# Optimization experiments

Measured on AMD Instinct MI355X. Metric: run time of the kernel, lower is better.

The kernel has to match this reference:

```python
import jax, jax.numpy as jnp
import numpy as np
from jax import lax

# dims: T steps, B batch, V vocab, E embed, H hidden, N cache slots, DK key dim, DV value dim
T, B, V, E, H, N, DK, DV = 64, 32, 32000, 512, 512, 512, 256, 512


def setup_inputs() -> dict:
    key = jax.random.key(0)
    ks = jax.random.split(key, 12)
    rn = lambda i, shape, scale: jax.random.normal(ks[i], shape, jnp.float32) * scale
    return {
        "tokens": jax.random.randint(ks[0], (T, B), 0, V),
        "emb": rn(1, (V, E), 0.02),
        "Wq": rn(2, (E, DK), E ** -0.5),
        "Wk": rn(3, (E, DK), E ** -0.5),
        "Wv": rn(4, (H, DV), H ** -0.5),
        "Wh": rn(5, (E + DV, H), (E + DV) ** -0.5),
        "bh": jnp.zeros((H,), jnp.float32),
        "Wout": rn(6, (H, V), H ** -0.5),
        "bout": jnp.zeros((V,), jnp.float32),
        "keys0": rn(7, (N, DK), 0.02),
        "values0": rn(8, (N, DV), 0.02),
        "k": 8,
    }


def reference(tokens, emb, Wq, Wk, Wv, Wh, bh, Wout, bout, keys0, values0, k):
    scale = 1.0 / jnp.sqrt(jnp.float32(DK))

    def step(carry, tok_t):
        keys, vals, ptr = carry
        x = emb[tok_t]                                  # [B, E] embedding gather
        q = x @ Wq                                      # [B, DK]
        scores = (q @ keys.T) * scale                   # [B, N]
        top_s, top_i = lax.top_k(scores, k)             # [B, k]
        w = jax.nn.softmax(top_s, axis=-1)              # [B, k]
        v_sel = vals[top_i]                             # [B, k, DV] irregular gather
        retrieved = jnp.einsum('bk,bkd->bd', w, v_sel)  # [B, DV]
        h = jnp.tanh(jnp.concatenate([x, retrieved], axis=-1) @ Wh + bh)  # [B, H]
        # circular-pointer cache write (batch-pooled key/value)
        new_key = jnp.mean(x @ Wk, axis=0)              # [DK]
        new_val = jnp.mean(h @ Wv, axis=0)              # [DV]
        keys = lax.dynamic_update_slice(keys, new_key[None, :], (ptr, 0))
        vals = lax.dynamic_update_slice(vals, new_val[None, :], (ptr, 0))
        ptr = (ptr + 1) % N
        return (keys, vals, ptr), h

    init = (keys0, values0, jnp.int32(0))
    _, hiddens = lax.scan(step, init, tokens)           # [T, B, H]
    logits = hiddens @ Wout + bout                      # [T, B, V]
    return logits
```

## Files before the change

kernel.cpp:

```cpp
#include <hip/hip_runtime.h>

typedef _Float16 half_t;
typedef _Float16 half8 __attribute__((ext_vector_type(8)));
typedef float f32x4 __attribute__((ext_vector_type(4)));


__device__ __forceinline__ void gload_lds16(const void* g, void* l) {
  __builtin_amdgcn_global_load_lds((const __attribute__((address_space(1))) void*)g,
                                   (__attribute__((address_space(3))) void*)l, 16, 0, 0);
}

__device__ __forceinline__ void prepTile(int pid, const float* __restrict__ Wout,
                                         half_t* __restrict__ WoutT,
                                         const float* __restrict__ Wh,
                                         half_t* __restrict__ W1T,
                                         half_t* __restrict__ W2T,
                                         char* smem) {
  half_t (*tile)[68] = (half_t(*)[68])smem;
  if (pid < 4000) {
    int n0 = (pid % 500) * 64, k0 = (pid / 500) * 64;
    for (int p = 0; p < 4; p++) {
      int id = p * 256 + threadIdx.x;
      int k = id >> 4, nq = id & 15;
      float4 v = *(const float4*)&Wout[(size_t)(k0 + k) * 32000 + n0 + nq * 4];
      tile[nq * 4 + 0][k] = (half_t)v.x; tile[nq * 4 + 1][k] = (half_t)v.y;
      tile[nq * 4 + 2][k] = (half_t)v.z; tile[nq * 4 + 3][k] = (half_t)v.w;
    }
    __syncthreads();
    for (int p = 0; p < 2; p++) {
      int id = p * 256 + threadIdx.x;
      int n = id >> 3, kc = id & 7;
      half8 h = *(const half8*)&tile[n][kc * 8];
      *(half8*)&WoutT[(size_t)(n0 + n) * 512 + k0 + kc * 8] = h;
    }
  } else {
    int id2 = pid - 4000;
    int n0 = (id2 & 7) * 64, k0 = (id2 >> 3) * 64;
    for (int p = 0; p < 16; p++) {
      int id = p * 256 + threadIdx.x;
      int kk = id >> 6, nn = id & 63;
      tile[nn][kk] = (half_t)Wh[(size_t)(k0 + kk) * 512 + n0 + nn];
    }
    __syncthreads();
    half_t* out = (k0 < 512) ? W1T : W2T;
    int kb = k0 & 511;
    for (int p = 0; p < 16; p++) {
      int id = p * 256 + threadIdx.x;
      int nn = id >> 6, kk = id & 63;
      out[(size_t)(n0 + nn) * 512 + kb + kk] = tile[nn][kk];
    }
  }
}

__global__ __launch_bounds__(256) void kGE(const int* __restrict__ tok,
                                           const float* __restrict__ emb,
                                           const float* __restrict__ Wq,
                                           const float* __restrict__ Wk,
                                           double* __restrict__ Qd,
                                           float* __restrict__ Q32,
                                           half_t* __restrict__ Xh,
                                           double* __restrict__ NKd,
                                           float* __restrict__ NKf) {
  __shared__ __align__(16) char smem[8192];
  int bid = blockIdx.x, tid = threadIdx.x;
  if (bid < 512) {
    float (*xs)[512] = (float(*)[512])smem;
    int r0 = bid * 4;
    for (int rr = 0; rr < 4; rr++) {
      int row = r0 + rr;
      const float* src = emb + (size_t)tok[row] * 512;
      float v0 = src[tid], v1 = src[tid + 256];
      xs[rr][tid] = v0; xs[rr][tid + 256] = v1;
      Xh[(size_t)row * 512 + tid] = (half_t)v0;
      Xh[(size_t)row * 512 + tid + 256] = (half_t)v1;
    }
    __syncthreads();
    int d = tid;
    double a0 = 0, a1 = 0, a2 = 0, a3 = 0;
    #pragma unroll 4
    for (int i = 0; i < 512; i++) {
      double w = (double)Wq[(size_t)i * 256 + d];
      a0 += (double)xs[0][i] * w; a1 += (double)xs[1][i] * w;
      a2 += (double)xs[2][i] * w; a3 += (double)xs[3][i] * w;
    }
    Qd[(size_t)(r0 + 0) * 256 + d] = a0; Qd[(size_t)(r0 + 1) * 256 + d] = a1;
    Qd[(size_t)(r0 + 2) * 256 + d] = a2; Qd[(size_t)(r0 + 3) * 256 + d] = a3;
    Q32[(size_t)(r0 + 0) * 256 + d] = (float)a0; Q32[(size_t)(r0 + 1) * 256 + d] = (float)a1;
    Q32[(size_t)(r0 + 2) * 256 + d] = (float)a2; Q32[(size_t)(r0 + 3) * 256 + d] = (float)a3;
  } else {
    double* xm = (double*)smem;
    int bid2 = bid - 512, t = bid2 >> 3, ch = bid2 & 7;
    int c = tid;
    double s0 = 0.0, s1 = 0.0;
    for (int b = 0; b < 32; b++) {
      const float* src = emb + (size_t)tok[t * 32 + b] * 512;
      s0 += (double)src[c]; s1 += (double)src[c + 256];
    }
    xm[c] = s0 * (1.0 / 32.0);
    xm[c + 256] = s1 * (1.0 / 32.0);
    __syncthreads();
    if (tid < 32) {
      int d = ch * 32 + tid;
      double a = 0;
      #pragma unroll 4
      for (int i = 0; i < 512; i++) a += xm[i] * (double)Wk[(size_t)i * 256 + d];
      NKd[(size_t)t * 256 + d] = a;
      NKf[(size_t)t * 256 + d] = (float)a;
    }
  }
}

__global__ __launch_bounds__(256) void kSP(const float* __restrict__ Q32,
                                           const float* __restrict__ keys0,
                                           const float* __restrict__ NKf,
                                           float* __restrict__ S,
                                           const float* __restrict__ Wout,
                                           half_t* __restrict__ WoutT,
                                           const float* __restrict__ Wh,
                                           half_t* __restrict__ W1T,
                                           half_t* __restrict__ W2T,
                                           int* __restrict__ DEP,
                                           int* __restrict__ bars) {
  __shared__ __align__(16) char smem[17408];
  int b = blockIdx.x, tid = threadIdx.x;
  if (b < 288) {
    float (*As)[68] = (float(*)[68])smem;
    float (*Bs)[68] = (float(*)[68])(smem + 8704);
    int m0 = (b & 31) * 64, n0 = (b >> 5) * 64;
    int tx = tid & 15, ty = tid >> 4;
    float acc[4][4];
    #pragma unroll
    for (int i = 0; i < 4; i++)
      #pragma unroll
      for (int j = 0; j < 4; j++) acc[i][j] = 0.f;
    for (int kc = 0; kc < 256; kc += 32) {
      __syncthreads();
      #pragma unroll
      for (int p = 0; p < 8; p++) {
        int idx = p * 256 + tid;
        int k = idx & 31, m = idx >> 5;
        As[k][m] = Q32[(size_t)(m0 + m) * 256 + kc + k];
        int n = n0 + m;
        Bs[k][m] = (n < 512) ? keys0[(size_t)n * 256 + kc + k]
                             : NKf[(size_t)(n - 512) * 256 + kc + k];
      }
      __syncthreads();
      #pragma unroll
      for (int k = 0; k < 32; k++) {
        float4 a = *(const float4*)&As[k][ty * 4];
        float4 bb = *(const float4*)&Bs[k][tx * 4];
        acc[0][0] += a.x * bb.x; acc[0][1] += a.x * bb.y; acc[0][2] += a.x * bb.z; acc[0][3] += a.x * bb.w;
        acc[1][0] += a.y * bb.x; acc[1][1] += a.y * bb.y; acc[1][2] += a.y * bb.z; acc[1][3] += a.y * bb.w;
        acc[2][0] += a.z * bb.x; acc[2][1] += a.z * bb.y; acc[2][2] += a.z * bb.z; acc[2][3] += a.z * bb.w;
        acc[3][0] += a.w * bb.x; acc[3][1] += a.w * bb.y; acc[3][2] += a.w * bb.z; acc[3][3] += a.w * bb.w;
      }
    }
    #pragma unroll
    for (int i = 0; i < 4; i++) {
      float4 o = {acc[i][0], acc[i][1], acc[i][2], acc[i][3]};
      *(float4*)&S[(size_t)(m0 + ty * 4 + i) * 576 + n0 + tx * 4] = o;
    }
  } else if (b < 2288) {
    prepTile(b - 288, Wout, WoutT, Wh, W1T, W2T, smem);
  } else {
    if (tid < 64) DEP[tid] = 0;
    bars[tid] = 0;
  }
}

__global__ __launch_bounds__(256) void kTR(const float* __restrict__ S,
                                           const double* __restrict__ Qd,
                                           const double* __restrict__ NKd,
                                           const float* __restrict__ keys0,
                                           const float* __restrict__ vals0,
                                           float* __restrict__ WSo,
                                           int* __restrict__ ISo,
                                           half_t* __restrict__ R16,
                                           int* __restrict__ DEP,
                                           const float* __restrict__ Wout,
                                           half_t* __restrict__ WoutT,
                                           const float* __restrict__ Wh,
                                           half_t* __restrict__ W1T,
                                           half_t* __restrict__ W2T) {
  __shared__ __align__(16) char smem[8704];
  int bid = blockIdx.x, tid = threadIdx.x;
  if (bid >= 512) {
    prepTile(2000 + (bid - 512), Wout, WoutT, Wh, W1T, W2T, smem);
    return;
  }
  __shared__ float wls[4][8];
  __shared__ int ils[4][8];
  __shared__ int depf;
  if (tid == 0) depf = 0;
  __syncthreads();
  int r0b = bid * 4;
  int wv = tid >> 6, lane = tid & 63;
  int row = r0b + wv;
  int t = row >> 5;
  const float* Srow = S + (size_t)row * 576;
  float v[8];
  #pragma unroll
  for (int j = 0; j < 8; j++) v[j] = Srow[j * 64 + lane];
  if (lane < t) v[0] = Srow[512 + lane];
  int ci[12];
  #pragma unroll
  for (int it = 0; it < 12; it++) {
    float bv = -1e30f; int bi = 0x7fffffff;
    #pragma unroll
    for (int j = 0; j < 8; j++) {
      int ii = j * 64 + lane;
      if (v[j] > bv || (v[j] == bv && ii < bi)) { bv = v[j]; bi = ii; }
    }
    #pragma unroll
    for (int s = 32; s > 0; s >>= 1) {
      float ov = __shfl_xor(bv, s, 64);
      int oi = __shfl_xor(bi, s, 64);
      if (ov > bv || (ov == bv && oi < bi)) { bv = ov; bi = oi; }
    }
    ci[it] = bi;
    #pragma unroll
    for (int j = 0; j < 8; j++)
      if (j * 64 + lane == bi) v[j] = -1e30f;
  }
  const double* qrow = Qd + (size_t)row * 256 + lane * 4;
  double q0 = qrow[0], q1 = qrow[1], q2 = qrow[2], q3 = qrow[3];
  double dv[12];
  #pragma unroll
  for (int c = 0; c < 12; c++) {
    int idx = ci[c];
    double p;
    if (idx < t) {
      const double* kr = NKd + (size_t)idx * 256 + lane * 4;
      p = q0 * kr[0] + q1 * kr[1] + q2 * kr[2] + q3 * kr[3];
    } else {
      const float* kr = keys0 + (size_t)idx * 256 + lane * 4;
      p = q0 * (double)kr[0] + q1 * (double)kr[1] + q2 * (double)kr[2] + q3 * (double)kr[3];
    }
    #pragma unroll
    for (int s = 32; s > 0; s >>= 1) p += __shfl_xor(p, s, 64);
    dv[c] = p * 0.0625;
  }
  double tv[8]; int ti[8];
  #pragma unroll
  for (int it = 0; it < 8; it++) {
    double bv = -1e300; int bi = 0x7fffffff;
    #pragma unroll
    for (int c = 0; c < 12; c++)
      if (dv[c] > bv || (dv[c] == bv && ci[c] < bi)) { bv = dv[c]; bi = ci[c]; }
    tv[it] = bv; ti[it] = bi;
    #pragma unroll
    for (int c = 0; c < 12; c++)
      if (ci[c] == bi) dv[c] = -1e300;
  }
  if (lane == 0) {
    double m = tv[0], ev[8], Z = 0;
    #pragma unroll
    for (int i2 = 0; i2 < 8; i2++) { ev[i2] = exp(tv[i2] - m); Z += ev[i2]; }
    double inv = 1.0 / Z;
    int dep = 0;
    #pragma unroll
    for (int i2 = 0; i2 < 8; i2++) {
      float w = (float)(ev[i2] * inv);
      WSo[(size_t)row * 8 + i2] = w;
      ISo[(size_t)row * 8 + i2] = ti[i2];
      wls[wv][i2] = w; ils[wv][i2] = ti[i2];
      if (ti[i2] < t) dep = 1;
    }
    if (dep) atomicOr(&depf, 1);
  }
  __syncthreads();
  if (tid == 0 && depf) atomicOr(&DEP[t], 1);
  for (int rr = 0; rr < 4; rr++) {
    float a0 = 0.f, a1 = 0.f;
    #pragma unroll
    for (int k2 = 0; k2 < 8; k2++) {
      const float* src = vals0 + (size_t)ils[rr][k2] * 512;
      a0 += wls[rr][k2] * src[tid];
      a1 += wls[rr][k2] * src[tid + 256];
    }
    R16[(size_t)(r0b + rr) * 512 + tid] = (half_t)a0;
    R16[(size_t)(r0b + rr) * 512 + tid + 256] = (half_t)a1;
  }
}

__device__ __forceinline__ void gbar(int* bars, int id, int nwg) {
  __syncthreads();
  if (threadIdx.x == 0) {
    __hip_atomic_fetch_add(&bars[id], 1, __ATOMIC_ACQ_REL, __HIP_MEMORY_SCOPE_AGENT);
    while (__hip_atomic_load(&bars[id], __ATOMIC_ACQUIRE, __HIP_MEMORY_SCOPE_AGENT) < nwg)
      __builtin_amdgcn_s_sleep(4);
  }
  __syncthreads();
}

__global__ __launch_bounds__(256) void kH(const half_t* __restrict__ Xh,
                                          const half_t* __restrict__ R16,
                                          const half_t* __restrict__ W1T,
                                          const half_t* __restrict__ W2T,
                                          const float* __restrict__ bh,
                                          const float* __restrict__ Wv,
                                          float* __restrict__ XH,
                                          half_t* __restrict__ HH,
                                          float* __restrict__ HM,
                                          float* __restrict__ NV,
                                          int* __restrict__ bars) {
  __shared__ half_t lA[3][64 * 32];
  __shared__ half_t lB[3][64 * 32];
  __shared__ float hmld[512];
  int b = blockIdx.x;
  int m0 = (b >> 3) * 64, n0 = (b & 7) * 64;
  int tid = threadIdx.x, wid = tid >> 6, lane = tid & 63;
  int wm = wid >> 1, wn = wid & 1;
  f32x4 acc[2][2];
  #pragma unroll
  for (int i = 0; i < 2; i++)
    #pragma unroll
    for (int j = 0; j < 2; j++) acc[i][j] = (f32x4){0.f, 0.f, 0.f, 0.f};
  int rA = lane >> 2;
  int cswz = ((lane & 3) ^ ((lane >> 3) & 3)) * 8;
  int koffs = (((lane >> 4) ^ ((lane >> 1) & 3))) * 8;
  auto issue = [&](int j, int buf) {
    const half_t* Ap = (j < 16) ? Xh : R16;
    const half_t* Bp = (j < 16) ? W1T : W2T;
    int kk = j & 15;
    gload_lds16(Ap + ((size_t)(m0 + wid * 16 + rA) * 512 + kk * 32 + cswz), (void*)(&lA[buf][wid * 512]));
    gload_lds16(Bp + ((size_t)(n0 + wid * 16 + rA) * 512 + kk * 32 + cswz), (void*)(&lB[buf][wid * 512]));
  };
  issue(0, 0); issue(1, 1);
  for (int kt = 0; kt < 32; kt++) {
    if (kt < 31) asm volatile("s_waitcnt vmcnt(2)\n\ts_barrier" ::: "memory");
    else         asm volatile("s_waitcnt vmcnt(0)\n\ts_barrier" ::: "memory");
    int cur = kt % 3;
    half8 af[2], bf[2];
    #pragma unroll
    for (int mf = 0; mf < 2; mf++)
      af[mf] = *(const half8*)&lA[cur][(wm * 32 + mf * 16 + (lane & 15)) * 32 + koffs];
    #pragma unroll
    for (int nf = 0; nf < 2; nf++)
      bf[nf] = *(const half8*)&lB[cur][(wn * 32 + nf * 16 + (lane & 15)) * 32 + koffs];
    if (kt < 30) issue(kt + 2, (kt + 2) % 3);
    #pragma unroll
    for (int mf = 0; mf < 2; mf++)
      #pragma unroll
      for (int nf = 0; nf < 2; nf++)
        acc[mf][nf] = __builtin_amdgcn_mfma_f32_16x16x32_f16(af[mf], bf[nf], acc[mf][nf], 0, 0, 0);
    if (kt == 15) {
      #pragma unroll
      for (int nf = 0; nf < 2; nf++) {
        int col = n0 + wn * 32 + nf * 16 + (lane & 15);
        float bv = bh[col];
        #pragma unroll
        for (int mf = 0; mf < 2; mf++) {
          int rbase = m0 + wm * 32 + mf * 16 + (lane >> 4) * 4;
          #pragma unroll
          for (int r = 0; r < 4; r++)
            XH[(size_t)(rbase + r) * 512 + col] = acc[mf][nf][r] + bv;
        }
      }
    }
  }
  #pragma unroll
  for (int nf = 0; nf < 2; nf++) {
    int col = n0 + wn * 32 + nf * 16 + (lane & 15);
    float bv = bh[col];
    float cs = 0.f;
    #pragma unroll
    for (int mf = 0; mf < 2; mf++) {
      int rbase = m0 + wm * 32 + mf * 16 + (lane >> 4) * 4;
      #pragma unroll
      for (int r = 0; r < 4; r++) {
        float v = tanhf(acc[mf][nf][r] + bv);
        HH[(size_t)(rbase + r) * 512 + col] = (half_t)v;
        cs += v;
      }
    }
    cs += __shfl_xor(cs, 16, 64);
    cs += __shfl_xor(cs, 32, 64);
    if ((lane >> 4) == 0) {
      int t = (m0 >> 5) + wm;
      HM[(size_t)t * 512 + col] = cs * (1.f / 32.f);
    }
  }
  gbar(bars, 0, 256);
  int t2 = b >> 2, ch = b & 3;
  hmld[tid] = HM[(size_t)t2 * 512 + tid];
  hmld[tid + 256] = HM[(size_t)t2 * 512 + tid + 256];
  __syncthreads();
  if (tid < 128) {
    int col = ch * 128 + tid;
    float a = 0.f;
    #pragma unroll 4
    for (int i = 0; i < 512; i++) a += hmld[i] * Wv[(size_t)i * 512 + col];
    NV[(size_t)t2 * 512 + col] = a;
  }
}

__global__ __launch_bounds__(256) void kFixup(const int* __restrict__ DEP,
                                              int* __restrict__ bars,
                                              const float* __restrict__ XHm,
                                              const float* __restrict__ Wh,
                                              const float* __restrict__ Wv,
                                              const float* __restrict__ vals0,
                                              const float* __restrict__ WSo,
                                              const int* __restrict__ ISo,
                                              float* __restrict__ NV,
                                              float* __restrict__ RETR,
                                              float* __restrict__ HB,
                                              half_t* __restrict__ HHm) {
  __shared__ float rl[512];
  __shared__ float hm2[512];
  int w = blockIdx.x;
  int barid = 0;
  for (int t = 0; t < 64; t++) {
    if (DEP[t] == 0) continue;
    {
      int b = w >> 1, hf = w & 1;
      int c = hf * 256 + threadIdx.x;
      int row = t * 32 + b;
      float acc = 0.f;
      #pragma unroll
      for (int k2 = 0; k2 < 8; k2++) {
        int idx = ISo[(size_t)row * 8 + k2];
        float wv2 = WSo[(size_t)row * 8 + k2];
        const float* src = (idx < t) ? (NV + (size_t)idx * 512) : (vals0 + (size_t)idx * 512);
        acc += wv2 * src[c];
      }
      RETR[(size_t)b * 512 + c] = acc;
    }
    gbar(bars, barid++, 64);
    if (w < 32) {
      int b = w;
      rl[threadIdx.x] = RETR[(size_t)b * 512 + threadIdx.x];
      rl[threadIdx.x + 256] = RETR[(size_t)b * 512 + threadIdx.x + 256];
      __syncthreads();
      int row = t * 32 + b;
      for (int cc = 0; cc < 2; cc++) {
        int col = cc * 256 + threadIdx.x;
        float acc = 0.f;
        #pragma unroll 4
        for (int i = 0; i < 512; i++) acc += rl[i] * Wh[(size_t)(512 + i) * 512 + col];
        float h = tanhf(XHm[(size_t)row * 512 + col] + acc);
        HB[(size_t)b * 512 + col] = h;
        HHm[(size_t)row * 512 + col] = (half_t)h;
      }
    }
    gbar(bars, barid++, 64);
    if (w == 0) {
      for (int j = threadIdx.x; j < 512; j += 256) {
        float s = 0.f;
        for (int b = 0; b < 32; b++) s += HB[(size_t)b * 512 + j];
        hm2[j] = s * (1.f / 32.f);
      }
      __syncthreads();
      for (int v = threadIdx.x; v < 512; v += 256) {
        float a = 0.f;
        #pragma unroll 4
        for (int i = 0; i < 512; i++) a += hm2[i] * Wv[(size_t)i * 512 + v];
        NV[(size_t)t * 512 + v] = a;
      }
    }
    gbar(bars, barid++, 64);
  }
}

__global__ __launch_bounds__(256) void kLogits(const half_t* __restrict__ A,
                                               const half_t* __restrict__ Bm,
                                               const float* __restrict__ bout,
                                               float* __restrict__ C) {
  __shared__ half_t lA[3][128 * 32];
  __shared__ half_t lB[3][128 * 32];
  int lin = blockIdx.y * 250 + blockIdx.x;
  int swz = (lin & 7) * 500 + (lin >> 3);
  int m0 = (swz & 15) * 128;
  int n0 = (swz >> 4) * 128;
  int tid = threadIdx.x, wid = tid >> 6, lane = tid & 63;
  int wm = wid >> 1, wn = wid & 1;
  f32x4 acc[4][4];
  #pragma unroll
  for (int a2 = 0; a2 < 4; a2++)
    #pragma unroll
    for (int b2 = 0; b2 < 4; b2++) acc[a2][b2] = (f32x4){0.f, 0.f, 0.f, 0.f};
  int rA = lane >> 2;
  int cswz = ((lane & 3) ^ ((lane >> 3) & 3)) * 8;
  int koffs = (((lane >> 4) ^ ((lane >> 1) & 3))) * 8;
  auto issue = [&](int j, int buf) {
    #pragma unroll
    for (int i2 = 0; i2 < 2; i2++) {
      int blk = wid * 2 + i2;
      gload_lds16(A + ((size_t)(m0 + blk * 16 + rA) * 512 + j * 32 + cswz), (void*)(&lA[buf][blk * 512]));
      gload_lds16(Bm + ((size_t)(n0 + blk * 16 + rA) * 512 + j * 32 + cswz), (void*)(&lB[buf][blk * 512]));
    }
  };
  issue(0, 0); issue(1, 1);
  for (int kt = 0; kt < 16; kt++) {
    if (kt < 15) asm volatile("s_waitcnt vmcnt(4)\n\ts_barrier" ::: "memory");
    else         asm volatile("s_waitcnt vmcnt(0)\n\ts_barrier" ::: "memory");
    int cur = kt % 3;
    half8 af[4], bf[4];
    #pragma unroll
    for (int mf = 0; mf < 4; mf++)
      af[mf] = *(const half8*)&lA[cur][(wm * 64 + mf * 16 + (lane & 15)) * 32 + koffs];
    #pragma unroll
    for (int nf = 0; nf < 4; nf++)
      bf[nf] = *(const half8*)&lB[cur][(wn * 64 + nf * 16 + (lane & 15)) * 32 + koffs];
    if (kt < 14) issue(kt + 2, (kt + 2) % 3);
    #pragma unroll
    for (int mf = 0; mf < 4; mf++)
      #pragma unroll
      for (int nf = 0; nf < 4; nf++)
        acc[mf][nf] = __builtin_amdgcn_mfma_f32_16x16x32_f16(af[mf], bf[nf], acc[mf][nf], 0, 0, 0);
  }
  #pragma unroll
  for (int nf = 0; nf < 4; nf++) {
    int col = n0 + wn * 64 + nf * 16 + (lane & 15);
    float bv = bout[col];
    #pragma unroll
    for (int mf = 0; mf < 4; mf++) {
      int rbase = m0 + wm * 64 + mf * 16 + (lane >> 4) * 4;
      #pragma unroll
      for (int r = 0; r < 4; r++)
        C[(size_t)(rbase + r) * 32000 + col] = acc[mf][nf][r] + bv;
    }
  }
}

extern "C" void kernel_launch(void* const* d_in, const int* in_sizes, int n_in,
                              void* d_out, int out_size, void* d_ws, size_t ws_size,
                              hipStream_t stream) {
  (void)in_sizes; (void)n_in; (void)out_size; (void)ws_size;
  const int*   tok   = (const int*)d_in[0];
  const float* emb   = (const float*)d_in[1];
  const float* Wq    = (const float*)d_in[2];
  const float* Wk    = (const float*)d_in[3];
  const float* Wv    = (const float*)d_in[4];
  const float* Wh    = (const float*)d_in[5];
  const float* bh    = (const float*)d_in[6];
  const float* Wout  = (const float*)d_in[7];
  const float* bout  = (const float*)d_in[8];
  const float* keys0 = (const float*)d_in[9];
  const float* vals0 = (const float*)d_in[10];
  float* Cout = (float*)d_out;

  char* ws = (char*)d_ws;
  size_t off = 0;
  auto alloc = [&](size_t bytes) -> char* {
    char* p = ws + off;
    off += (bytes + 255) & ~(size_t)255;
    return p;
  };
  half_t* WoutT = (half_t*)alloc(32768000);
  half_t* W1T   = (half_t*)alloc(524288);
  half_t* W2T   = (half_t*)alloc(524288);
  half_t* Xh    = (half_t*)alloc(2097152);
  double* Qd    = (double*)alloc(4194304);
  float*  Q32   = (float*) alloc(2097152);
  double* NKd   = (double*)alloc(131072);
  float*  NKf   = (float*) alloc(65536);
  float*  Sb    = (float*) alloc(4718592);
  float*  XH    = (float*) alloc(4194304);
  float*  WSb   = (float*) alloc(65536);
  int*    ISb   = (int*)   alloc(65536);
  float*  NV    = (float*) alloc(131072);
  half_t* R16   = (half_t*)alloc(2097152);
  half_t* HH    = (half_t*)alloc(2097152);
  float*  HM    = (float*) alloc(131072);
  float*  RETR  = (float*) alloc(65536);
  float*  HB    = (float*) alloc(65536);
  int*    DEP   = (int*)   alloc(256);
  int*    bars  = (int*)   alloc(1024);

  kGE<<<1024, 256, 0, stream>>>(tok, emb, Wq, Wk, Qd, Q32, Xh, NKd, NKf);
  kSP<<<2289, 256, 0, stream>>>(Q32, keys0, NKf, Sb, Wout, WoutT, Wh, W1T, W2T, DEP, bars);
  kTR<<<2640, 256, 0, stream>>>(Sb, Qd, NKd, keys0, vals0, WSb, ISb, R16, DEP,
                                Wout, WoutT, Wh, W1T, W2T);
  kH<<<256, 256, 0, stream>>>(Xh, R16, W1T, W2T, bh, Wv, XH, HH, HM, NV, bars);
  kFixup<<<64, 256, 0, stream>>>(DEP, bars + 16, XH, Wh, Wv, vals0, WSb, ISb, NV, RETR, HB, HH);
  kLogits<<<dim3(250, 16), 256, 0, stream>>>(HH, WoutT, bout, Cout);
}
```

Before: 328.0 us.

## Move all weight prep into first kernel and stage logits epilogue through LDS

All weight transpose/convert tiles (Wout, Wh) and the DEP/bars reset now run as extra blocks of the first embedding kernel instead of being spread across the score and top-k kernels, which shrink to just their real work. The logits GEMM epilogue now writes accumulators into LDS in two halves and then emits coalesced float4 stores with a vectorised bias add, replacing scattered scalar stores. This rebalances the work across kernels and improves store coalescing on the largest output, at the cost of extra barriers and LDS traffic in the epilogue. It also puts the prep work into one large front-loaded grid.

```diff
diff --git a/kernel.cpp b/kernel.cpp
--- a/kernel.cpp
+++ b/kernel.cpp
@@ -60,9 +60,21 @@
                                            float* __restrict__ Q32,
                                            half_t* __restrict__ Xh,
                                            double* __restrict__ NKd,
-                                           float* __restrict__ NKf) {
-  __shared__ __align__(16) char smem[8192];
+                                           float* __restrict__ NKf,
+                                           const float* __restrict__ Wout,
+                                           half_t* __restrict__ WoutT,
+                                           const float* __restrict__ Wh,
+                                           half_t* __restrict__ W1T,
+                                           half_t* __restrict__ W2T,
+                                           int* __restrict__ DEP,
+                                           int* __restrict__ bars) {
+  __shared__ __align__(16) char smem[8704];
   int bid = blockIdx.x, tid = threadIdx.x;
+  if (bid >= 1024) {
+    if (bid < 5152) prepTile(bid - 1024, Wout, WoutT, Wh, W1T, W2T, smem);
+    else { if (tid < 64) DEP[tid] = 0; bars[tid] = 0; }
+    return;
+  }
   if (bid < 512) {
     float (*xs)[512] = (float(*)[512])smem;
     int r0 = bid * 4;
@@ -110,61 +122,46 @@
   }
 }
 
-__global__ __launch_bounds__(256) void kSP(const float* __restrict__ Q32,
-                                           const float* __restrict__ keys0,
-                                           const float* __restrict__ NKf,
-                                           float* __restrict__ S,
-                                           const float* __restrict__ Wout,
-                                           half_t* __restrict__ WoutT,
-                                           const float* __restrict__ Wh,
-                                           half_t* __restrict__ W1T,
-                                           half_t* __restrict__ W2T,
-                                           int* __restrict__ DEP,
-                                           int* __restrict__ bars) {
-  __shared__ __align__(16) char smem[17408];
+__global__ __launch_bounds__(256) void kS(const float* __restrict__ Q32,
+                                          const float* __restrict__ keys0,
+                                          const float* __restrict__ NKf,
+                                          float* __restrict__ S) {
+  __shared__ float As[32][68];
+  __shared__ float Bs[32][68];
   int b = blockIdx.x, tid = threadIdx.x;
-  if (b < 288) {
-    float (*As)[68] = (float(*)[68])smem;
-    float (*Bs)[68] = (float(*)[68])(smem + 8704);
-    int m0 = (b & 31) * 64, n0 = (b >> 5) * 64;
-    int tx = tid & 15, ty = tid >> 4;
-    float acc[4][4];
-    #pragma unroll
-    for (int i = 0; i < 4; i++)
-      #pragma unroll
-      for (int j = 0; j < 4; j++) acc[i][j] = 0.f;
-    for (int kc = 0; kc < 256; kc += 32) {
-      __syncthreads();
-      #pragma unroll
-      for (int p = 0; p < 8; p++) {
-        int idx = p * 256 + tid;
-        int k = idx & 31, m = idx >> 5;
-        As[k][m] = Q32[(size_t)(m0 + m) * 256 + kc + k];
-        int n = n0 + m;
-        Bs[k][m] = (n < 512) ? keys0[(size_t)n * 256 + kc + k]
-                             : NKf[(size_t)(n - 512) * 256 + kc + k];
-      }
-      __syncthreads();
-      #pragma unroll
-      for (int k = 0; k < 32; k++) {
-        float4 a = *(const float4*)&As[k][ty * 4];
-        float4 bb = *(const float4*)&Bs[k][tx * 4];
-        acc[0][0] += a.x * bb.x; acc[0][1] += a.x * bb.y; acc[0][2] += a.x * bb.z; acc[0][3] += a.x * bb.w;
-        acc[1][0] += a.y * bb.x; acc[1][1] += a.y * bb.y; acc[1][2] += a.y * bb.z; acc[1][3] += a.y * bb.w;
-        acc[2][0] += a.z * bb.x; acc[2][1] += a.z * bb.y; acc[2][2] += a.z * bb.z; acc[2][3] += a.z * bb.w;
-        acc[3][0] += a.w * bb.x; acc[3][1] += a.w * bb.y; acc[3][2] += a.w * bb.z; acc[3][3] += a.w * bb.w;
-      }
-    }
-    #pragma unroll
-    for (int i = 0; i < 4; i++) {
-      float4 o = {acc[i][0], acc[i][1], acc[i][2], acc[i][3]};
-      *(float4*)&S[(size_t)(m0 + ty * 4 + i) * 576 + n0 + tx * 4] = o;
-    }
-  } else if (b < 2288) {
-    prepTile(b - 288, Wout, WoutT, Wh, W1T, W2T, smem);
-  } else {
-    if (tid < 64) DEP[tid] = 0;
-    bars[tid] = 0;
+  int m0 = (b & 31) * 64, n0 = (b >> 5) * 64;
+  int tx = tid & 15, ty = tid >> 4;
+  float acc[4][4];
+  #pragma unroll
+  for (int i = 0; i < 4; i++)
+    #pragma unroll
+    for (int j = 0; j < 4; j++) acc[i][j] = 0.f;
+  for (int kc = 0; kc < 256; kc += 32) {
+    __syncthreads();
+    #pragma unroll
+    for (int p = 0; p < 8; p++) {
+      int idx = p * 256 + tid;
+      int k = idx & 31, m = idx >> 5;
+      As[k][m] = Q32[(size_t)(m0 + m) * 256 + kc + k];
+      int n = n0 + m;
+      Bs[k][m] = (n < 512) ? keys0[(size_t)n * 256 + kc + k]
+                           : NKf[(size_t)(n - 512) * 256 + kc + k];
+    }
+    __syncthreads();
+    #pragma unroll
+    for (int k = 0; k < 32; k++) {
+      float4 a = *(const float4*)&As[k][ty * 4];
+      float4 bb = *(const float4*)&Bs[k][tx * 4];
+      acc[0][0] += a.x * bb.x; acc[0][1] += a.x * bb.y; acc[0][2] += a.x * bb.z; acc[0][3] += a.x * bb.w;
+      acc[1][0] += a.y * bb.x; acc[1][1] += a.y * bb.y; acc[1][2] += a.y * bb.z; acc[1][3] += a.y * bb.w;
+      acc[2][0] += a.z * bb.x; acc[2][1] += a.z * bb.y; acc[2][2] += a.z * bb.z; acc[2][3] += a.z * bb.w;
+      acc[3][0] += a.w * bb.x; acc[3][1] += a.w * bb.y; acc[3][2] += a.w * bb.z; acc[3][3] += a.w * bb.w;
+    }
+  }
+  #pragma unroll
+  for (int i = 0; i < 4; i++) {
+    float4 o = {acc[i][0], acc[i][1], acc[i][2], acc[i][3]};
+    *(float4*)&S[(size_t)(m0 + ty * 4 + i) * 576 + n0 + tx * 4] = o;
   }
 }
 
@@ -176,21 +173,11 @@
                                            float* __restrict__ WSo,
                                            int* __restrict__ ISo,
                                            half_t* __restrict__ R16,
-                                           int* __restrict__ DEP,
-                                           const float* __restrict__ Wout,
-                                           half_t* __restrict__ WoutT,
-                                           const float* __restrict__ Wh,
-                                           half_t* __restrict__ W1T,
-                                           half_t* __restrict__ W2T) {
-  __shared__ __align__(16) char smem[8704];
-  int bid = blockIdx.x, tid = threadIdx.x;
-  if (bid >= 512) {
-    prepTile(2000 + (bid - 512), Wout, WoutT, Wh, W1T, W2T, smem);
-    return;
-  }
+                                           int* __restrict__ DEP) {
   __shared__ float wls[4][8];
   __shared__ int ils[4][8];
   __shared__ int depf;
+  int bid = blockIdx.x, tid = threadIdx.x;
   if (tid == 0) depf = 0;
   __syncthreads();
   int r0b = bid * 4;
@@ -467,8 +454,9 @@
                                                const half_t* __restrict__ Bm,
                                                const float* __restrict__ bout,
                                                float* __restrict__ C) {
-  __shared__ half_t lA[3][128 * 32];
-  __shared__ half_t lB[3][128 * 32];
+  __shared__ __align__(16) char smem[49152];
+  half_t* lAb = (half_t*)smem;
+  half_t* lBb = (half_t*)(smem + 24576);
   int lin = blockIdx.y * 250 + blockIdx.x;
   int swz = (lin & 7) * 500 + (lin >> 3);
   int m0 = (swz & 15) * 128;
@@ -487,8 +475,8 @@
     #pragma unroll
     for (int i2 = 0; i2 < 2; i2++) {
       int blk = wid * 2 + i2;
-      gload_lds16(A + ((size_t)(m0 + blk * 16 + rA) * 512 + j * 32 + cswz), (void*)(&lA[buf][blk * 512]));
-      gload_lds16(Bm + ((size_t)(n0 + blk * 16 + rA) * 512 + j * 32 + cswz), (void*)(&lB[buf][blk * 512]));
+      gload_lds16(A + ((size_t)(m0 + blk * 16 + rA) * 512 + j * 32 + cswz), (void*)(lAb + buf * 4096 + blk * 512));
+      gload_lds16(Bm + ((size_t)(n0 + blk * 16 + rA) * 512 + j * 32 + cswz), (void*)(lBb + buf * 4096 + blk * 512));
     }
   };
   issue(0, 0); issue(1, 1);
@@ -499,10 +487,10 @@
     half8 af[4], bf[4];
     #pragma unroll
     for (int mf = 0; mf < 4; mf++)
-      af[mf] = *(const half8*)&lA[cur][(wm * 64 + mf * 16 + (lane & 15)) * 32 + koffs];
+      af[mf] = *(const half8*)(lAb + cur * 4096 + (wm * 64 + mf * 16 + (lane & 15)) * 32 + koffs);
     #pragma unroll
     for (int nf = 0; nf < 4; nf++)
-      bf[nf] = *(const half8*)&lB[cur][(wn * 64 + nf * 16 + (lane & 15)) * 32 + koffs];
+      bf[nf] = *(const half8*)(lBb + cur * 4096 + (wn * 64 + nf * 16 + (lane & 15)) * 32 + koffs);
     if (kt < 14) issue(kt + 2, (kt + 2) % 3);
     #pragma unroll
     for (int mf = 0; mf < 4; mf++)
@@ -510,16 +498,32 @@
       for (int nf = 0; nf < 4; nf++)
         acc[mf][nf] = __builtin_amdgcn_mfma_f32_16x16x32_f16(af[mf], bf[nf], acc[mf][nf], 0, 0, 0);
   }
-  #pragma unroll
-  for (int nf = 0; nf < 4; nf++) {
-    int col = n0 + wn * 64 + nf * 16 + (lane & 15);
-    float bv = bout[col];
-    #pragma unroll
-    for (int mf = 0; mf < 4; mf++) {
-      int rbase = m0 + wm * 64 + mf * 16 + (lane >> 4) * 4;
+  float (*cst)[128] = (float(*)[128])smem;
+  #pragma unroll
+  for (int half = 0; half < 2; half++) {
+    __syncthreads();
+    if (wm == half) {
       #pragma unroll
-      for (int r = 0; r < 4; r++)
-        C[(size_t)(rbase + r) * 32000 + col] = acc[mf][nf][r] + bv;
+      for (int nf = 0; nf < 4; nf++) {
+        int col = wn * 64 + nf * 16 + (lane & 15);
+        #pragma unroll
+        for (int mf = 0; mf < 4; mf++) {
+          int rr = mf * 16 + (lane >> 4) * 4;
+          #pragma unroll
+          for (int r = 0; r < 4; r++)
+            cst[rr + r][col] = acc[mf][nf][r];
+        }
+      }
+    }
+    __syncthreads();
+    #pragma unroll
+    for (int p = 0; p < 8; p++) {
+      int idx = p * 256 + tid;
+      int rr = idx >> 5, cc = idx & 31;
+      float4 v = *(float4*)&cst[rr][cc * 4];
+      const float4 bv = *(const float4*)&bout[n0 + cc * 4];
+      v.x += bv.x; v.y += bv.y; v.z += bv.z; v.w += bv.w;
+      *(float4*)&C[(size_t)(m0 + half * 64 + rr) * 32000 + n0 + cc * 4] = v;
     }
   }
 }
@@ -569,10 +573,10 @@
   int*    DEP   = (int*)   alloc(256);
   int*    bars  = (int*)   alloc(1024);
 
-  kGE<<<1024, 256, 0, stream>>>(tok, emb, Wq, Wk, Qd, Q32, Xh, NKd, NKf);
-  kSP<<<2289, 256, 0, stream>>>(Q32, keys0, NKf, Sb, Wout, WoutT, Wh, W1T, W2T, DEP, bars);
-  kTR<<<2640, 256, 0, stream>>>(Sb, Qd, NKd, keys0, vals0, WSb, ISb, R16, DEP,
-                                Wout, WoutT, Wh, W1T, W2T);
+  kGE<<<5153, 256, 0, stream>>>(tok, emb, Wq, Wk, Qd, Q32, Xh, NKd, NKf,
+                                Wout, WoutT, Wh, W1T, W2T, DEP, bars);
+  kS<<<288, 256, 0, stream>>>(Q32, keys0, NKf, Sb);
+  kTR<<<512, 256, 0, stream>>>(Sb, Qd, NKd, keys0, vals0, WSb, ISb, R16, DEP);
   kH<<<256, 256, 0, stream>>>(Xh, R16, W1T, W2T, bh, Wv, XH, HH, HM, NV, bars);
   kFixup<<<64, 256, 0, stream>>>(DEP, bars + 16, XH, Wh, Wv, vals0, WSb, ISb, NV, RETR, HB, HH);
   kLogits<<<dim3(250, 16), 256, 0, stream>>>(HH, WoutT, bout, Cout);
```

Result: slower. 335.5 us (+2.3%).
